# Kernel optimization log

Measured on AMD Instinct MI355X. Metric: run time of the kernel, lower is better.

Reference implementation:

```python
import jax, jax.numpy as jnp
import numpy as np

B, S, H = 2, 2048, 2048
NH, HD = 16, 128
I = 8192
EPS = float(np.finfo(np.float32).eps)  # torch RMSNorm default eps=None -> dtype eps


def rmsnorm(x, w):
    var = jnp.mean(jnp.square(x), axis=-1, keepdims=True)
    return x * jax.lax.rsqrt(var + EPS) * w


def setup_inputs() -> dict:
    key = jax.random.key(0)
    ks = jax.random.split(key, 8)
    s = 0.02
    return {
        "hidden_states": jax.random.normal(ks[0], (B, S, H), jnp.float32),
        "Wq": jax.random.normal(ks[1], (H, H), jnp.float32) * s,
        "Wk": jax.random.normal(ks[2], (H, H), jnp.float32) * s,
        "Wv": jax.random.normal(ks[3], (H, H), jnp.float32) * s,
        "Wo": jax.random.normal(ks[4], (H, H), jnp.float32) * s,
        "Wg": jax.random.normal(ks[5], (I, H), jnp.float32) * s,
        "Wu": jax.random.normal(ks[6], (I, H), jnp.float32) * s,
        "Wd": jax.random.normal(ks[7], (H, I), jnp.float32) * s,
        "g_in": jnp.ones((H,), jnp.float32),
        "g_post": jnp.ones((H,), jnp.float32),
    }


def reference(hidden_states, Wq, Wk, Wv, Wo, Wg, Wu, Wd, g_in, g_post):
    residual = hidden_states
    x = rmsnorm(hidden_states, g_in)
    # projections: nn.Linear does x @ W.T
    q = (x @ Wq.T).reshape(B, S, NH, HD).transpose(0, 2, 1, 3)  # [B,NH,S,HD]
    k = (x @ Wk.T).reshape(B, S, NH, HD).transpose(0, 2, 1, 3)
    v = (x @ Wv.T).reshape(B, S, NH, HD).transpose(0, 2, 1, 3)
    scores = jnp.einsum("bhqd,bhkd->bhqk", q, k) / jnp.sqrt(jnp.float32(HD))
    attn = jax.nn.softmax(scores, axis=-1)
    out = jnp.einsum("bhqk,bhkd->bhqd", attn, v)
    out = out.transpose(0, 2, 1, 3).reshape(B, S, H)
    hidden_states = residual + out @ Wo.T
    residual = hidden_states
    x = rmsnorm(hidden_states, g_post)
    mlp = (jax.nn.silu(x @ Wg.T) * (x @ Wu.T)) @ Wd.T
    return residual + mlp
```

## Files before the change

kernel.cpp:

```cpp
#include <hip/hip_runtime.h>

using u16 = unsigned short;
using u32 = unsigned int;

typedef __attribute__((ext_vector_type(8))) __bf16 bf16x8;
typedef __attribute__((ext_vector_type(4))) float f32x4;

__device__ __forceinline__ u16 f2bf(float f) {
  u32 u = __float_as_uint(f);
  u32 r = (u + 0x7fffu + ((u >> 16) & 1u)) >> 16;
  return (u16)r;
}
__device__ __forceinline__ u32 pk2(float a, float b) {
  return (u32)f2bf(a) | ((u32)f2bf(b) << 16);
}
__device__ __forceinline__ float bf2f(u16 h) {
  return __uint_as_float(((u32)h) << 16);
}
__device__ __forceinline__ void gload16(const u16* g, u16* l) {
  __builtin_amdgcn_global_load_lds((const __attribute__((address_space(1))) void*)g,
                                   (__attribute__((address_space(3))) void*)l, 16, 0, 0);
}
__device__ __forceinline__ f32x4 mfma_bf16(bf16x8 a, bf16x8 b, f32x4 c) {
  return __builtin_amdgcn_mfma_f32_16x16x32_bf16(a, b, c, 0, 0, 0);
}

__global__ __launch_bounds__(256) void cvt_bf16(const float* __restrict__ in,
                                                u16* __restrict__ out, int n8) {
  int i = blockIdx.x * 256 + threadIdx.x;
  int stride = gridDim.x * 256;
  for (; i < n8; i += stride) {
    float4 a = ((const float4*)in)[(size_t)i * 2];
    float4 b = ((const float4*)in)[(size_t)i * 2 + 1];
    ((uint4*)out)[i] = make_uint4(pk2(a.x, a.y), pk2(a.z, a.w), pk2(b.x, b.y), pk2(b.z, b.w));
  }
}

__global__ __launch_bounds__(256) void rmsnorm_bf16(const float* __restrict__ x,
                                                    const float* __restrict__ g,
                                                    u16* __restrict__ o) {
  const int row = blockIdx.x;
  const int tid = threadIdx.x;
  const float4* xr = (const float4*)(x + (size_t)row * 2048);
  float4 a = xr[tid * 2], b = xr[tid * 2 + 1];
  float s = a.x * a.x + a.y * a.y + a.z * a.z + a.w * a.w +
            b.x * b.x + b.y * b.y + b.z * b.z + b.w * b.w;
#pragma unroll
  for (int off = 1; off < 64; off <<= 1) s += __shfl_xor(s, off);
  __shared__ float red[4];
  if ((tid & 63) == 0) red[tid >> 6] = s;
  __syncthreads();
  s = red[0] + red[1] + red[2] + red[3];
  const float r = rsqrtf(s * (1.0f / 2048.0f) + 1.1920929e-07f);
  const float4* gr = (const float4*)g;
  float4 ga = gr[tid * 2], gb = gr[tid * 2 + 1];
  ((uint4*)(o + (size_t)row * 2048))[tid] =
      make_uint4(pk2(a.x * r * ga.x, a.y * r * ga.y), pk2(a.z * r * ga.z, a.w * r * ga.w),
                 pk2(b.x * r * gb.x, b.y * r * gb.y), pk2(b.z * r * gb.z, b.w * r * gb.w));
}

template <int EPI, int BN, int WM, int WN>
__global__ __launch_bounds__(512, 2) void gemm256(const u16* __restrict__ A,
                                                  const u16* __restrict__ B,
                                                  u16* Cb, float* Cf, const float* __restrict__ Res,
                                                  int M, int N, int K, int lda) {
  constexpr int NBH = BN / 128;
  constexpr int MR = 256 / WM / 16;
  constexpr int NR = BN / WN / 16;
  constexpr int HALF = 8192;
  alignas(16) __shared__ u16 lds[2][(2 + NBH) * HALF];

  const int tid = threadIdx.x;
  const int w = tid >> 6, lane = tid & 63;
  const int lo = lane & 15, hi = lane >> 4;

  const int nwg = gridDim.x;
  const int swz = (blockIdx.x & 7) * (nwg >> 3) + (blockIdx.x >> 3);
  const int nbx = N / BN;
  const int bm = (swz / nbx) * 256, bn = (swz % nbx) * BN;

  const int wm = w / WN, wn = w % WN;
  const int WRB = wm * (256 / WM), WCB = wn * (BN / WN);
  const int ah = WRB >> 7, arb = WRB & 127;
  const int bh = WCB >> 7, brb = WCB & 127;

  const int trow = tid >> 3, twin = tid & 7;
  const int scol = (twin ^ (trow & 7)) * 8;
  const u16* Ag = A + (size_t)(bm + trow) * lda + scol;
  const u16* Bg = B + (size_t)(bn + trow) * K + scol;

  f32x4 acc[MR][NR] = {};

#define STAGE(Ld, kt)                                                              \
  {                                                                                \
    _Pragma("unroll") for (int hc = 0; hc < 4; ++hc)                               \
        gload16(Ag + (size_t)(hc * 64) * lda + (kt), (Ld) + hc * 4096 + tid * 8);  \
    _Pragma("unroll") for (int hc = 0; hc < NBH * 2; ++hc)                         \
        gload16(Bg + (size_t)(hc * 64) * K + (kt), (Ld) + (2 + 0) * HALF + hc * 4096 + tid * 8); \
  }

  STAGE(&lds[0][0], 0);
  __syncthreads();
  int cur = 0;
  for (int kt = 0; kt < K; kt += 64) {
    if (kt + 64 < K) STAGE(&lds[cur ^ 1][0], kt + 64);
    const u16* LA = &lds[cur][0] + ah * HALF;
    const u16* LB = &lds[cur][0] + (2 + bh) * HALF;
#pragma unroll
    for (int ks = 0; ks < 2; ++ks) {
      const int pw = ((ks << 2) | hi) ^ (lo & 7);
      bf16x8 af[MR], bf[NR];
#pragma unroll
      for (int m = 0; m < MR; ++m)
        af[m] = *(const bf16x8*)(LA + (arb + m * 16 + lo) * 64 + pw * 8);
#pragma unroll
      for (int n = 0; n < NR; ++n)
        bf[n] = *(const bf16x8*)(LB + (brb + n * 16 + lo) * 64 + pw * 8);
      __builtin_amdgcn_s_setprio(1);
#pragma unroll
      for (int m = 0; m < MR; ++m)
#pragma unroll
        for (int n = 0; n < NR; ++n) acc[m][n] = mfma_bf16(af[m], bf[n], acc[m][n]);
      __builtin_amdgcn_s_setprio(0);
    }
    __syncthreads();
    cur ^= 1;
  }
#undef STAGE

#pragma unroll
  for (int m = 0; m < MR; ++m) {
    const int gr = bm + WRB + m * 16 + hi * 4;
#pragma unroll
    for (int n = 0; n < NR; ++n) {
      const int gc = bn + WCB + n * 16 + lo;
#pragma unroll
      for (int r = 0; r < 4; ++r) {
        const size_t idx = (size_t)(gr + r) * N + gc;
        if constexpr (EPI == 1) {
          Cf[idx] = Res[idx] + acc[m][n][r];
        } else if constexpr (EPI == 2) {
          float g = bf2f(Cb[idx]);
          float s = g / (1.f + __expf(-g));
          Cb[idx] = f2bf(s * acc[m][n][r]);
        } else {
          Cb[idx] = f2bf(acc[m][n][r]);
        }
      }
    }
  }
}

template <int EPI>
__global__ __launch_bounds__(256) void gemm_bt(const u16* __restrict__ A,
                                               const float* __restrict__ B,
                                               u16* Cb, float* Cf, const float* Res,
                                               int M, int N, int K) {
  alignas(16) __shared__ u16 As[128 * 32];
  alignas(16) __shared__ u16 Bs[128 * 32];
  const int tid = threadIdx.x;
  const int w = tid >> 6, lane = tid & 63;
  const int lo = lane & 15, hi = lane >> 4;
  const int bm = blockIdx.y * 128, bn = blockIdx.x * 128;
  const int wr = (w >> 1) * 64, wc = (w & 1) * 64;
  f32x4 acc[4][4] = {};
  const int r0 = tid >> 2, kc0 = (tid & 3) * 8;
  const u16* a0 = A + (size_t)(bm + r0) * K + kc0;
  const u16* a1 = A + (size_t)(bm + 64 + r0) * K + kc0;
  const float* b0 = B + (size_t)(bn + r0) * K + kc0;
  const float* b1 = B + (size_t)(bn + 64 + r0) * K + kc0;
  u16* asd0 = &As[(size_t)tid * 8];
  u16* asd1 = &As[(size_t)(tid + 256) * 8];
  u16* bsd0 = &Bs[(size_t)tid * 8];
  u16* bsd1 = &Bs[(size_t)(tid + 256) * 8];
  for (int kt = 0; kt < K; kt += 32) {
    gload16(a0 + kt, asd0);
    gload16(a1 + kt, asd1);
    float4 x0 = *(const float4*)(b0 + kt);
    float4 x1 = *(const float4*)(b0 + kt + 4);
    float4 y0 = *(const float4*)(b1 + kt);
    float4 y1 = *(const float4*)(b1 + kt + 4);
    *(uint4*)bsd0 = make_uint4(pk2(x0.x, x0.y), pk2(x0.z, x0.w), pk2(x1.x, x1.y), pk2(x1.z, x1.w));
    *(uint4*)bsd1 = make_uint4(pk2(y0.x, y0.y), pk2(y0.z, y0.w), pk2(y1.x, y1.y), pk2(y1.z, y1.w));
    __syncthreads();
    bf16x8 af[4], bfr[4];
#pragma unroll
    for (int i = 0; i < 4; ++i) {
      af[i] = *(const bf16x8*)(&As[(wr + i * 16 + lo) * 32 + hi * 8]);
      bfr[i] = *(const bf16x8*)(&Bs[(wc + i * 16 + lo) * 32 + hi * 8]);
    }
#pragma unroll
    for (int i = 0; i < 4; ++i)
#pragma unroll
      for (int j = 0; j < 4; ++j) acc[i][j] = mfma_bf16(af[i], bfr[j], acc[i][j]);
    __syncthreads();
  }
#pragma unroll
  for (int i = 0; i < 4; ++i) {
    const int gr = bm + wr + i * 16 + hi * 4;
#pragma unroll
    for (int j = 0; j < 4; ++j) {
      const int gc = bn + wc + j * 16 + lo;
#pragma unroll
      for (int r = 0; r < 4; ++r) {
        const size_t idx = (size_t)(gr + r) * N + gc;
        if constexpr (EPI == 1) {
          Cf[idx] = Res[idx] + acc[i][j][r];
        } else if constexpr (EPI == 2) {
          float g = bf2f(Cb[idx]);
          float s = g / (1.f + __expf(-g));
          Cb[idx] = f2bf(s * acc[i][j][r]);
        } else {
          Cb[idx] = f2bf(acc[i][j][r]);
        }
      }
    }
  }
}

__global__ __launch_bounds__(256) void transpose_v(const u16* __restrict__ v,
                                                   u16* __restrict__ vt, int ldv) {
  __shared__ u16 t[32][33];
  const int bh = blockIdx.z, b = bh >> 4, h = bh & 15;
  const int s0 = blockIdx.x * 32, d0 = blockIdx.y * 32;
  const int tx = threadIdx.x, ty = threadIdx.y;
#pragma unroll
  for (int i = 0; i < 4; ++i)
    t[ty + i * 8][tx] = v[(size_t)(b * 2048 + s0 + ty + i * 8) * ldv + h * 128 + d0 + tx];
  __syncthreads();
#pragma unroll
  for (int i = 0; i < 4; ++i)
    vt[(size_t)(bh * 128 + d0 + ty + i * 8) * 2048 + s0 + tx] = t[tx][ty + i * 8];
}

__global__ __launch_bounds__(256) void attn_fwd2(const u16* __restrict__ q,
                                                 const u16* __restrict__ k,
                                                 const u16* __restrict__ vt,
                                                 u16* o, int ldq) {
  constexpr int S = 2048;
  alignas(16) __shared__ u16 Ks[2][64 * 128];
  alignas(16) __shared__ u16 Vs[2][128 * 64];
  alignas(16) __shared__ u16 plds[4][16 * 72];
  const int bh = blockIdx.y, b = bh >> 4, h = bh & 15;
  const int tid = threadIdx.x, w = tid >> 6, lane = tid & 63;
  const int lo = lane & 15, hi = lane >> 4;
  const int qr = blockIdx.x * 64 + w * 16;
  u16* pl = &plds[w][0];

  bf16x8 qf[4];
  const u16* qb = q + (size_t)(b * S + qr + lo) * ldq + h * 128 + hi * 8;
#pragma unroll
  for (int ks = 0; ks < 4; ++ks) qf[ks] = *(const bf16x8*)(qb + ks * 32);

  f32x4 oacc[8] = {};
  float m[4], l[4];
#pragma unroll
  for (int r = 0; r < 4; ++r) { m[r] = -1e30f; l[r] = 0.f; }

  const u16* kb = k + (size_t)(b * S) * ldq + h * 128;
  const u16* vb = vt + (size_t)bh * 128 * S;

  const int kcs = ((((tid & 15) * 16) ^ (((tid >> 4) & 7) << 4)) >> 1);
  const int vcs = ((((tid & 7) * 16) ^ (((tid >> 3) & 7) << 4)) >> 1);
  const u16* kgs = kb + (size_t)(tid >> 4) * ldq + kcs;
  const u16* vgs = vb + (size_t)(tid >> 3) * S + vcs;

  int cur = 0;
#pragma unroll
  for (int c = 0; c < 4; ++c) gload16(kgs + (size_t)(c * 16) * ldq, &Ks[0][c * 2048 + tid * 8]);
#pragma unroll
  for (int c = 0; c < 4; ++c) gload16(vgs + (size_t)(c * 32) * S, &Vs[0][c * 2048 + tid * 8]);
  __syncthreads();

  const int swq = (lo & 7) << 4;

  for (int kv = 0; kv < S; kv += 64) {
    if (kv + 64 < S) {
      const int nb = cur ^ 1;
#pragma unroll
      for (int c = 0; c < 4; ++c)
        gload16(kgs + (size_t)(kv + 64 + c * 16) * ldq, &Ks[nb][c * 2048 + tid * 8]);
#pragma unroll
      for (int c = 0; c < 4; ++c)
        gload16(vgs + (size_t)(c * 32) * S + kv + 64, &Vs[nb][c * 2048 + tid * 8]);
    }
    const u16* Kc = &Ks[cur][0];
    const u16* Vc = &Vs[cur][0];

    f32x4 sacc[4] = {};
    __builtin_amdgcn_s_setprio(1);
#pragma unroll
    for (int ks = 0; ks < 4; ++ks)
#pragma unroll
      for (int n = 0; n < 4; ++n) {
        bf16x8 kf = *(const bf16x8*)(Kc + (n * 16 + lo) * 128 + (((ks * 64 + hi * 16) ^ swq) >> 1));
        sacc[n] = mfma_bf16(qf[ks], kf, sacc[n]);
      }
    __builtin_amdgcn_s_setprio(0);

    constexpr float sc = 0.08838834764831845f;
    constexpr float L2E = 1.4426950408889634f;
#pragma unroll
    for (int n = 0; n < 4; ++n) sacc[n] = sacc[n] * sc;
    float mv[4];
#pragma unroll
    for (int r = 0; r < 4; ++r)
      mv[r] = fmaxf(fmaxf(sacc[0][r], sacc[1][r]), fmaxf(sacc[2][r], sacc[3][r]));
#pragma unroll
    for (int off = 1; off < 16; off <<= 1)
#pragma unroll
      for (int r = 0; r < 4; ++r) mv[r] = fmaxf(mv[r], __shfl_xor(mv[r], off));
    float corr[4];
#pragma unroll
    for (int r = 0; r < 4; ++r) {
      float mn = fmaxf(m[r], mv[r]);
      corr[r] = exp2f((m[r] - mn) * L2E);
      m[r] = mn;
    }
    f32x4 p[4];
#pragma unroll
    for (int n = 0; n < 4; ++n)
#pragma unroll
      for (int r = 0; r < 4; ++r) p[n][r] = exp2f((sacc[n][r] - m[r]) * L2E);
    float ps[4];
#pragma unroll
    for (int r = 0; r < 4; ++r) ps[r] = p[0][r] + p[1][r] + p[2][r] + p[3][r];
#pragma unroll
    for (int off = 1; off < 16; off <<= 1)
#pragma unroll
      for (int r = 0; r < 4; ++r) ps[r] += __shfl_xor(ps[r], off);
#pragma unroll
    for (int r = 0; r < 4; ++r) l[r] = l[r] * corr[r] + ps[r];
#pragma unroll
    for (int f = 0; f < 8; ++f)
#pragma unroll
      for (int r = 0; r < 4; ++r) oacc[f][r] *= corr[r];

#pragma unroll
    for (int n = 0; n < 4; ++n)
#pragma unroll
      for (int r = 0; r < 4; ++r)
        pl[(hi * 4 + r) * 72 + n * 16 + lo] = f2bf(p[n][r]);
    asm volatile("s_waitcnt lgkmcnt(0)" ::: "memory");
    bf16x8 pf0 = *(const bf16x8*)(pl + lo * 72 + hi * 8);
    bf16x8 pf1 = *(const bf16x8*)(pl + lo * 72 + 32 + hi * 8);

    __builtin_amdgcn_s_setprio(1);
#pragma unroll
    for (int f = 0; f < 8; ++f) {
      const int row = f * 16 + lo;
      bf16x8 vf0 = *(const bf16x8*)(Vc + row * 64 + (((hi * 16) ^ swq) >> 1));
      bf16x8 vf1 = *(const bf16x8*)(Vc + row * 64 + (((64 + hi * 16) ^ swq) >> 1));
      oacc[f] = mfma_bf16(pf0, vf0, oacc[f]);
      oacc[f] = mfma_bf16(pf1, vf1, oacc[f]);
    }
    __builtin_amdgcn_s_setprio(0);

    __syncthreads();
    cur ^= 1;
  }

  u16* ob = o + (size_t)(b * S + qr) * ldq + h * 128;
#pragma unroll
  for (int f = 0; f < 8; ++f)
#pragma unroll
    for (int r = 0; r < 4; ++r)
      ob[(size_t)(hi * 4 + r) * ldq + f * 16 + lo] = f2bf(oacc[f][r] / l[r]);
}

extern "C" void kernel_launch(void* const* d_in, const int* in_sizes, int n_in,
                              void* d_out, int out_size, void* d_ws, size_t ws_size,
                              hipStream_t stream) {
  constexpr int B = 2, S = 2048, H = 2048, NH = 16, I = 8192;
  constexpr int M = B * S;

  const float* hs = (const float*)d_in[0];
  const float* Wq = (const float*)d_in[1];
  const float* Wk = (const float*)d_in[2];
  const float* Wv = (const float*)d_in[3];
  const float* Wo = (const float*)d_in[4];
  const float* Wg = (const float*)d_in[5];
  const float* Wu = (const float*)d_in[6];
  const float* Wd = (const float*)d_in[7];
  const float* g_in = (const float*)d_in[8];
  const float* g_post = (const float*)d_in[9];
  float* out = (float*)d_out;

  constexpr size_t SZ_HH = (size_t)H * H * 2;
  constexpr size_t SZ_IH = (size_t)I * H * 2;
  constexpr size_t SZ_MH = (size_t)M * H * 2;
  constexpr size_t NEED_NEW = SZ_MH + 3 * SZ_MH + SZ_MH + SZ_IH;

  if (ws_size >= NEED_NEW) {
    char* p = (char*)d_ws;
    u16* x_b = (u16*)p;    p += SZ_MH;
    u16* qkv_b = (u16*)p;  p += 3 * SZ_MH;
    u16* vt_b = (u16*)p;   p += SZ_MH;
    u16* wsc = (u16*)p;    p += SZ_IH;
    u16* gate_b = qkv_b;

    rmsnorm_bf16<<<M, 256, 0, stream>>>(hs, g_in, x_b);

    cvt_bf16<<<1024, 256, 0, stream>>>(Wq, wsc, H * H / 8);
    cvt_bf16<<<1024, 256, 0, stream>>>(Wk, wsc + (size_t)H * H, H * H / 8);
    cvt_bf16<<<1024, 256, 0, stream>>>(Wv, wsc + (size_t)2 * H * H, H * H / 8);
    gemm256<0, 256, 2, 4><<<(M / 256) * (3 * H / 256), 512, 0, stream>>>(
        x_b, wsc, qkv_b, nullptr, nullptr, M, 3 * H, H, H);

    transpose_v<<<dim3(S / 32, 128 / 32, B * NH), dim3(32, 8), 0, stream>>>(
        qkv_b + 2 * H, vt_b, 3 * H);
    attn_fwd2<<<dim3(S / 64, B * NH), 256, 0, stream>>>(qkv_b, qkv_b + H, vt_b, qkv_b, 3 * H);

    cvt_bf16<<<1024, 256, 0, stream>>>(Wo, wsc, H * H / 8);
    gemm256<1, 128, 4, 2><<<(M / 256) * (H / 128), 512, 0, stream>>>(
        qkv_b, wsc, nullptr, out, hs, M, H, H, 3 * H);

    rmsnorm_bf16<<<M, 256, 0, stream>>>(out, g_post, x_b);

    cvt_bf16<<<1024, 256, 0, stream>>>(Wg, wsc, I * H / 8);
    gemm256<0, 256, 2, 4><<<(M / 256) * (I / 256), 512, 0, stream>>>(
        x_b, wsc, gate_b, nullptr, nullptr, M, I, H, H);
    cvt_bf16<<<1024, 256, 0, stream>>>(Wu, wsc, I * H / 8);
    gemm256<2, 256, 2, 4><<<(M / 256) * (I / 256), 512, 0, stream>>>(
        x_b, wsc, gate_b, nullptr, nullptr, M, I, H, H);
    cvt_bf16<<<1024, 256, 0, stream>>>(Wd, wsc, I * H / 8);
    gemm256<1, 128, 4, 2><<<(M / 256) * (H / 128), 512, 0, stream>>>(
        gate_b, wsc, nullptr, out, out, M, H, I, I);
    return;
  }

  constexpr int MC = 2048;
  char* p = (char*)d_ws;
  u16* x_b = (u16*)p;   p += SZ_MH;
  u16* q_b = (u16*)p;   p += SZ_MH;
  u16* k_b = (u16*)p;   p += SZ_MH;
  u16* v_b = (u16*)p;   p += SZ_MH;
  u16* vt_b = (u16*)p;  p += SZ_MH;
  u16* g_mlp = k_b;

  rmsnorm_bf16<<<M, 256, 0, stream>>>(hs, g_in, x_b);
  const dim3 gHH(H / 128, M / 128);
  gemm_bt<0><<<gHH, 256, 0, stream>>>(x_b, Wq, q_b, nullptr, nullptr, M, H, H);
  gemm_bt<0><<<gHH, 256, 0, stream>>>(x_b, Wk, k_b, nullptr, nullptr, M, H, H);
  gemm_bt<0><<<gHH, 256, 0, stream>>>(x_b, Wv, v_b, nullptr, nullptr, M, H, H);
  transpose_v<<<dim3(S / 32, 128 / 32, B * NH), dim3(32, 8), 0, stream>>>(v_b, vt_b, H);
  attn_fwd2<<<dim3(S / 64, B * NH), 256, 0, stream>>>(q_b, k_b, vt_b, q_b, H);
  gemm_bt<1><<<gHH, 256, 0, stream>>>(q_b, Wo, nullptr, out, hs, M, H, H);
  rmsnorm_bf16<<<M, 256, 0, stream>>>(out, g_post, x_b);
  const dim3 gIH(I / 128, MC / 128), gHI(H / 128, MC / 128);
  for (int mc = 0; mc < M / MC; ++mc) {
    const u16* xc = x_b + (size_t)mc * MC * H;
    float* oc = out + (size_t)mc * MC * H;
    gemm_bt<0><<<gIH, 256, 0, stream>>>(xc, Wg, g_mlp, nullptr, nullptr, MC, I, H);
    gemm_bt<2><<<gIH, 256, 0, stream>>>(xc, Wu, g_mlp, nullptr, nullptr, MC, I, H);
    gemm_bt<1><<<gHI, 256, 0, stream>>>(g_mlp, Wd, nullptr, oc, oc, MC, H, I);
  }
}
```

Before: 871.0 us.

## Add 8-phase interleaved GEMM and lazy softmax rescaling in attention

Introduces a new 256x256 GEMM kernel that splits each 64-wide K tile into two halves and interleaves LDS fragment reads, async global-to-LDS prefetch of the next tile, and MFMA clusters across barrier-separated phases. It is used for the QKV, gate and up projections. Attention now folds the scale and log2e into one constant with an fma, and only rescales the running max, sum and output accumulators when a row's max grows past a threshold, skipping most correction multiplies. The bf16 conversion switches to the compiler's native cast. The trade-off is many more barriers per iteration, tighter vmcnt bookkeeping, and a softmax whose max can lag behind the true row max.

```diff
diff --git a/kernel.cpp b/kernel.cpp
--- a/kernel.cpp
+++ b/kernel.cpp
@@ -7,9 +7,8 @@
 typedef __attribute__((ext_vector_type(4))) float f32x4;
 
 __device__ __forceinline__ u16 f2bf(float f) {
-  u32 u = __float_as_uint(f);
-  u32 r = (u + 0x7fffu + ((u >> 16) & 1u)) >> 16;
-  return (u16)r;
+  __bf16 h = (__bf16)f;
+  return __builtin_bit_cast(u16, h);
 }
 __device__ __forceinline__ u32 pk2(float a, float b) {
   return (u32)f2bf(a) | ((u32)f2bf(b) << 16);
@@ -59,6 +58,148 @@
                  pk2(b.x * r * gb.x, b.y * r * gb.y), pk2(b.z * r * gb.z, b.w * r * gb.w));
 }
 
+template <int EPI>
+__global__ __launch_bounds__(512, 2) void gemm8p(const u16* __restrict__ A,
+                                                 const u16* __restrict__ B,
+                                                 u16* Cb, float* Cf,
+                                                 const float* __restrict__ Res,
+                                                 int M, int N, int K, int lda) {
+  alignas(16) __shared__ u16 lds[2 * 32768];
+  const int tid = threadIdx.x;
+  const int w = tid >> 6, lane = tid & 63;
+  const int lo = lane & 15, hi = lane >> 4;
+  const int nwg = gridDim.x;
+  const int swz = (blockIdx.x & 7) * (nwg >> 3) + (blockIdx.x >> 3);
+  const int nbx = N >> 8;
+  const int bm = (swz / nbx) << 8, bn = (swz % nbx) << 8;
+  const int wm = w >> 2, wn = w & 3;
+
+  const int pw = (hi ^ (lo & 3)) * 8;
+  const int arow = wm * 128 + lo;
+  const int brow = wn * 64 + lo;
+
+  const int srow = tid >> 2;
+  const int slw = ((tid & 3) ^ (srow & 3)) * 8;
+  const u16* Ag = A + (size_t)(bm + srow) * lda + slw;
+  const u16* Bg = B + (size_t)(bn + srow) * K + slw;
+
+  f32x4 acc[8][4] = {};
+
+#define AOFF(buf, kh) ((buf) * 32768 + (kh) * 8192)
+#define BOFF(buf, kh) ((buf) * 32768 + 16384 + (kh) * 8192)
+#define STG_A(buf, kh, kt)                                                        \
+  {                                                                               \
+    gload16(Ag + (kt) + (kh) * 32, &lds[AOFF(buf, kh) + tid * 8]);                \
+    gload16(Ag + (size_t)128 * lda + (kt) + (kh) * 32,                            \
+            &lds[AOFF(buf, kh) + 4096 + tid * 8]);                                \
+  }
+#define STG_B(buf, kh, kt)                                                        \
+  {                                                                               \
+    gload16(Bg + (kt) + (kh) * 32, &lds[BOFF(buf, kh) + tid * 8]);                \
+    gload16(Bg + (size_t)128 * K + (kt) + (kh) * 32,                              \
+            &lds[BOFF(buf, kh) + 4096 + tid * 8]);                                \
+  }
+
+  STG_A(0, 0, 0); STG_B(0, 0, 0); STG_A(0, 1, 0); STG_B(0, 1, 0);
+  asm volatile("s_waitcnt vmcnt(0)" ::: "memory");
+  __builtin_amdgcn_s_barrier();
+
+  const int NT = K >> 6;
+  for (int T = 0; T < NT; ++T) {
+    const int cur = T & 1, nxt = cur ^ 1;
+    const int kt1 = (T + 1) << 6;
+    const bool pre = (T + 1 < NT);
+    const u16* LA0 = &lds[AOFF(cur, 0)];
+    const u16* LB0 = &lds[BOFF(cur, 0)];
+    const u16* LA1 = &lds[AOFF(cur, 1)];
+    const u16* LB1 = &lds[BOFF(cur, 1)];
+    bf16x8 af[4], bf[4];
+
+#pragma unroll
+    for (int n = 0; n < 4; ++n) bf[n] = *(const bf16x8*)(LB0 + (brow + n * 16) * 32 + pw);
+#pragma unroll
+    for (int m = 0; m < 4; ++m) af[m] = *(const bf16x8*)(LA0 + (arow + m * 16) * 32 + pw);
+    if (pre) STG_A(nxt, 0, kt1);
+    __builtin_amdgcn_s_barrier();
+    __builtin_amdgcn_s_setprio(1);
+#pragma unroll
+    for (int m = 0; m < 4; ++m)
+#pragma unroll
+      for (int n = 0; n < 4; ++n) acc[m][n] = mfma_bf16(af[m], bf[n], acc[m][n]);
+    __builtin_amdgcn_s_setprio(0);
+    __builtin_amdgcn_s_barrier();
+
+#pragma unroll
+    for (int m = 0; m < 4; ++m)
+      af[m] = *(const bf16x8*)(LA0 + (arow + (m + 4) * 16) * 32 + pw);
+    if (pre) STG_B(nxt, 0, kt1);
+    __builtin_amdgcn_s_barrier();
+    __builtin_amdgcn_s_setprio(1);
+#pragma unroll
+    for (int m = 0; m < 4; ++m)
+#pragma unroll
+      for (int n = 0; n < 4; ++n) acc[m + 4][n] = mfma_bf16(af[m], bf[n], acc[m + 4][n]);
+    __builtin_amdgcn_s_setprio(0);
+    if (pre) { asm volatile("s_waitcnt vmcnt(4)" ::: "memory"); }
+    else     { asm volatile("s_waitcnt vmcnt(0)" ::: "memory"); }
+    __builtin_amdgcn_s_barrier();
+
+#pragma unroll
+    for (int n = 0; n < 4; ++n) bf[n] = *(const bf16x8*)(LB1 + (brow + n * 16) * 32 + pw);
+#pragma unroll
+    for (int m = 0; m < 4; ++m) af[m] = *(const bf16x8*)(LA1 + (arow + m * 16) * 32 + pw);
+    if (pre) STG_A(nxt, 1, kt1);
+    __builtin_amdgcn_s_barrier();
+    __builtin_amdgcn_s_setprio(1);
+#pragma unroll
+    for (int m = 0; m < 4; ++m)
+#pragma unroll
+      for (int n = 0; n < 4; ++n) acc[m][n] = mfma_bf16(af[m], bf[n], acc[m][n]);
+    __builtin_amdgcn_s_setprio(0);
+    __builtin_amdgcn_s_barrier();
+
+#pragma unroll
+    for (int m = 0; m < 4; ++m)
+      af[m] = *(const bf16x8*)(LA1 + (arow + (m + 4) * 16) * 32 + pw);
+    if (pre) STG_B(nxt, 1, kt1);
+    __builtin_amdgcn_s_barrier();
+    __builtin_amdgcn_s_setprio(1);
+#pragma unroll
+    for (int m = 0; m < 4; ++m)
+#pragma unroll
+      for (int n = 0; n < 4; ++n) acc[m + 4][n] = mfma_bf16(af[m], bf[n], acc[m + 4][n]);
+    __builtin_amdgcn_s_setprio(0);
+    if (pre) { asm volatile("s_waitcnt vmcnt(4)" ::: "memory"); }
+    __builtin_amdgcn_s_barrier();
+  }
+#undef STG_A
+#undef STG_B
+#undef AOFF
+#undef BOFF
+
+#pragma unroll
+  for (int m = 0; m < 8; ++m) {
+    const int gr = bm + wm * 128 + m * 16 + hi * 4;
+#pragma unroll
+    for (int n = 0; n < 4; ++n) {
+      const int gc = bn + wn * 64 + n * 16 + lo;
+#pragma unroll
+      for (int r = 0; r < 4; ++r) {
+        const size_t idx = (size_t)(gr + r) * N + gc;
+        if constexpr (EPI == 1) {
+          Cf[idx] = Res[idx] + acc[m][n][r];
+        } else if constexpr (EPI == 2) {
+          float g = bf2f(Cb[idx]);
+          float s = g / (1.f + __expf(-g));
+          Cb[idx] = f2bf(s * acc[m][n][r]);
+        } else {
+          Cb[idx] = f2bf(acc[m][n][r]);
+        }
+      }
+    }
+  }
+}
+
 template <int EPI, int BN, int WM, int WN>
 __global__ __launch_bounds__(512, 2) void gemm256(const u16* __restrict__ A,
                                                   const u16* __restrict__ B,
@@ -73,12 +214,10 @@
   const int tid = threadIdx.x;
   const int w = tid >> 6, lane = tid & 63;
   const int lo = lane & 15, hi = lane >> 4;
-
   const int nwg = gridDim.x;
   const int swz = (blockIdx.x & 7) * (nwg >> 3) + (blockIdx.x >> 3);
   const int nbx = N / BN;
   const int bm = (swz / nbx) * 256, bn = (swz % nbx) * BN;
-
   const int wm = w / WN, wn = w % WN;
   const int WRB = wm * (256 / WM), WCB = wn * (BN / WN);
   const int ah = WRB >> 7, arb = WRB & 127;
@@ -96,7 +235,7 @@
     _Pragma("unroll") for (int hc = 0; hc < 4; ++hc)                               \
         gload16(Ag + (size_t)(hc * 64) * lda + (kt), (Ld) + hc * 4096 + tid * 8);  \
     _Pragma("unroll") for (int hc = 0; hc < NBH * 2; ++hc)                         \
-        gload16(Bg + (size_t)(hc * 64) * K + (kt), (Ld) + (2 + 0) * HALF + hc * 4096 + tid * 8); \
+        gload16(Bg + (size_t)(hc * 64) * K + (kt), (Ld) + 2 * HALF + hc * 4096 + tid * 8); \
   }
 
   STAGE(&lds[0][0], 0);
@@ -108,14 +247,14 @@
     const u16* LB = &lds[cur][0] + (2 + bh) * HALF;
 #pragma unroll
     for (int ks = 0; ks < 2; ++ks) {
-      const int pw = ((ks << 2) | hi) ^ (lo & 7);
+      const int pwv = ((ks << 2) | hi) ^ (lo & 7);
       bf16x8 af[MR], bf[NR];
 #pragma unroll
       for (int m = 0; m < MR; ++m)
-        af[m] = *(const bf16x8*)(LA + (arb + m * 16 + lo) * 64 + pw * 8);
+        af[m] = *(const bf16x8*)(LA + (arb + m * 16 + lo) * 64 + pwv * 8);
 #pragma unroll
       for (int n = 0; n < NR; ++n)
-        bf[n] = *(const bf16x8*)(LB + (brb + n * 16 + lo) * 64 + pw * 8);
+        bf[n] = *(const bf16x8*)(LB + (brb + n * 16 + lo) * 64 + pwv * 8);
       __builtin_amdgcn_s_setprio(1);
 #pragma unroll
       for (int m = 0; m < MR; ++m)
@@ -273,6 +412,7 @@
   __syncthreads();
 
   const int swq = (lo & 7) << 4;
+  constexpr float SCL = 0.12752956f;
 
   for (int kv = 0; kv < S; kv += 64) {
     if (kv + 64 < S) {
@@ -298,10 +438,6 @@
       }
     __builtin_amdgcn_s_setprio(0);
 
-    constexpr float sc = 0.08838834764831845f;
-    constexpr float L2E = 1.4426950408889634f;
-#pragma unroll
-    for (int n = 0; n < 4; ++n) sacc[n] = sacc[n] * sc;
     float mv[4];
 #pragma unroll
     for (int r = 0; r < 4; ++r)
@@ -310,31 +446,39 @@
     for (int off = 1; off < 16; off <<= 1)
 #pragma unroll
       for (int r = 0; r < 4; ++r) mv[r] = fmaxf(mv[r], __shfl_xor(mv[r], off));
-    float corr[4];
-#pragma unroll
-    for (int r = 0; r < 4; ++r) {
-      float mn = fmaxf(m[r], mv[r]);
-      corr[r] = exp2f((m[r] - mn) * L2E);
-      m[r] = mn;
-    }
+
+    bool need = false;
+#pragma unroll
+    for (int r = 0; r < 4; ++r) need = need || (mv[r] > m[r] + 62.f);
+    if (__any(need)) {
+#pragma unroll
+      for (int r = 0; r < 4; ++r) {
+        float nm = fmaxf(m[r], mv[r]);
+        float c = exp2f((m[r] - nm) * SCL);
+        m[r] = nm;
+        l[r] *= c;
+#pragma unroll
+        for (int f = 0; f < 8; ++f) oacc[f][r] *= c;
+      }
+    }
+    float mm[4];
+#pragma unroll
+    for (int r = 0; r < 4; ++r) mm[r] = m[r] * SCL;
+
     f32x4 p[4];
 #pragma unroll
     for (int n = 0; n < 4; ++n)
 #pragma unroll
-      for (int r = 0; r < 4; ++r) p[n][r] = exp2f((sacc[n][r] - m[r]) * L2E);
+      for (int r = 0; r < 4; ++r) p[n][r] = exp2f(fmaf(sacc[n][r], SCL, -mm[r]));
     float ps[4];
 #pragma unroll
-    for (int r = 0; r < 4; ++r) ps[r] = p[0][r] + p[1][r] + p[2][r] + p[3][r];
+    for (int r = 0; r < 4; ++r) ps[r] = (p[0][r] + p[1][r]) + (p[2][r] + p[3][r]);
 #pragma unroll
     for (int off = 1; off < 16; off <<= 1)
 #pragma unroll
       for (int r = 0; r < 4; ++r) ps[r] += __shfl_xor(ps[r], off);
 #pragma unroll
-    for (int r = 0; r < 4; ++r) l[r] = l[r] * corr[r] + ps[r];
-#pragma unroll
-    for (int f = 0; f < 8; ++f)
-#pragma unroll
-      for (int r = 0; r < 4; ++r) oacc[f][r] *= corr[r];
+    for (int r = 0; r < 4; ++r) l[r] += ps[r];
 
 #pragma unroll
     for (int n = 0; n < 4; ++n)
@@ -404,7 +548,7 @@
     cvt_bf16<<<1024, 256, 0, stream>>>(Wq, wsc, H * H / 8);
     cvt_bf16<<<1024, 256, 0, stream>>>(Wk, wsc + (size_t)H * H, H * H / 8);
     cvt_bf16<<<1024, 256, 0, stream>>>(Wv, wsc + (size_t)2 * H * H, H * H / 8);
-    gemm256<0, 256, 2, 4><<<(M / 256) * (3 * H / 256), 512, 0, stream>>>(
+    gemm8p<0><<<(M / 256) * (3 * H / 256), 512, 0, stream>>>(
         x_b, wsc, qkv_b, nullptr, nullptr, M, 3 * H, H, H);
 
     transpose_v<<<dim3(S / 32, 128 / 32, B * NH), dim3(32, 8), 0, stream>>>(
@@ -418,10 +562,10 @@
     rmsnorm_bf16<<<M, 256, 0, stream>>>(out, g_post, x_b);
 
     cvt_bf16<<<1024, 256, 0, stream>>>(Wg, wsc, I * H / 8);
-    gemm256<0, 256, 2, 4><<<(M / 256) * (I / 256), 512, 0, stream>>>(
+    gemm8p<0><<<(M / 256) * (I / 256), 512, 0, stream>>>(
         x_b, wsc, gate_b, nullptr, nullptr, M, I, H, H);
     cvt_bf16<<<1024, 256, 0, stream>>>(Wu, wsc, I * H / 8);
-    gemm256<2, 256, 2, 4><<<(M / 256) * (I / 256), 512, 0, stream>>>(
+    gemm8p<2><<<(M / 256) * (I / 256), 512, 0, stream>>>(
         x_b, wsc, gate_b, nullptr, nullptr, M, I, H, H);
     cvt_bf16<<<1024, 256, 0, stream>>>(Wd, wsc, I * H / 8);
     gemm256<1, 128, 4, 2><<<(M / 256) * (H / 128), 512, 0, stream>>>(
```

Result: slower. 916.9 us (+5.3%).
